# Performance work log

Hardware: AMD Instinct MI355X
Metric: run time of the kernel (lower is better)

The kernel has to match this reference:

```python
import jax, jax.numpy as jnp
import numpy as np

N_NODES = 100000
N_EDGES = 3200000
F_IN, F_HID, F_OUT = 512, 128, 32


def setup_inputs() -> dict:
    key = jax.random.key(0)
    ks = jax.random.split(key, 8)
    x = jax.random.normal(ks[0], (N_NODES, F_IN), dtype=jnp.float32)
    edge_row = jax.random.randint(ks[1], (N_EDGES,), 0, N_NODES, dtype=jnp.int32)
    edge_col = jax.random.randint(ks[2], (N_EDGES,), 0, N_NODES, dtype=jnp.int32)
    edge_val = jax.random.uniform(ks[3], (N_EDGES,), dtype=jnp.float32)
    W1 = jax.random.normal(ks[4], (F_IN, F_HID), dtype=jnp.float32) / np.sqrt(F_IN)
    b1 = jnp.zeros((F_HID,), dtype=jnp.float32)
    W2 = jax.random.normal(ks[5], (F_HID, F_OUT), dtype=jnp.float32) / np.sqrt(F_HID)
    b2 = jnp.zeros((F_OUT,), dtype=jnp.float32)
    return {"x": x, "edge_row": edge_row, "edge_col": edge_col,
            "edge_val": edge_val, "W1": W1, "b1": b1, "W2": W2, "b2": b2}


def _spmm(edge_row, edge_col, edge_val, dense):
    # out[r] = sum_{e: row[e]==r} val[e] * dense[col[e]]  (COO SpMM)
    gathered = dense[edge_col] * edge_val[:, None]  # [E, F]
    return jax.ops.segment_sum(gathered, edge_row, num_segments=N_NODES)


def reference(x, edge_row, edge_col, edge_val, W1, b1, W2, b2):
    # GraphConvolution 1: support = x@W1; out = A @ support + b1
    h = _spmm(edge_row, edge_col, edge_val, x @ W1) + b1
    h = jax.nn.relu(h)
    # GraphConvolution 2
    logits = _spmm(edge_row, edge_col, edge_val, h @ W2) + b2
    return jax.nn.log_softmax(logits, axis=1)
```

## Files before the change

kernel.cpp:

```cpp
#include <hip/hip_runtime.h>


#define NN 100000
#define NE 3200000
#define FIN 512
#define FHID 128
#define FOUT 32
#define BROWS 256
#define NBUCK 391
#define NPART 256
#define CHUNK 12800
#define TOT (NBUCK * NPART)
#define NSCAN1 98
#define GG1 ((NN + 127) / 128)

typedef __attribute__((ext_vector_type(8))) short bf16x8;
typedef __attribute__((ext_vector_type(4))) float f32x4;

static __device__ __forceinline__ unsigned short f2bf(float f) {
    unsigned u = __float_as_uint(f);
    unsigned r = (u + 0x7FFFu + ((u >> 16) & 1u)) >> 16;
    return (unsigned short)r;
}
static __device__ __forceinline__ float bf2f(unsigned short u) {
    return __uint_as_float(((unsigned)u) << 16);
}
static __device__ __forceinline__ float bflo(unsigned u) {
    return __uint_as_float(u << 16);
}
static __device__ __forceinline__ float bfhi(unsigned u) {
    return __uint_as_float(u & 0xffff0000u);
}

__global__ __launch_bounds__(256) void fused_prep_hist(const float* __restrict__ W1,
                                                       unsigned short* __restrict__ W1t,
                                                       const int* __restrict__ erow,
                                                       int* __restrict__ cntG) {
    if (blockIdx.x < NPART) {
        __shared__ int c[NBUCK];
        const int t = threadIdx.x;
        const int w = blockIdx.x;
        for (int i = t; i < NBUCK; i += 256) c[i] = 0;
        __syncthreads();
        const int e0 = w * CHUNK;
        const int e1 = min(e0 + CHUNK, NE);
        for (int e = e0 + t; e < e1; e += 256) atomicAdd(&c[erow[e] >> 8], 1);
        __syncthreads();
        for (int i = t; i < NBUCK; i += 256) cntG[w * NBUCK + i] = c[i];
    } else {
        int t = (blockIdx.x - NPART) * 256 + threadIdx.x;
        int n = t & 127;
        int k = t >> 7;
        W1t[n * 512 + k] = f2bf(W1[k * 128 + n]);
    }
}

__global__ __launch_bounds__(256) void scan1_kernel(const int* __restrict__ cntG,
                                                    int* __restrict__ off,
                                                    int* __restrict__ partials) {
    __shared__ int s[256];
    int t = threadIdx.x;
    int i0 = blockIdx.x * 1024 + t * 4;
    int v[4];
#pragma unroll
    for (int j = 0; j < 4; ++j) {
        int i = i0 + j;
        v[j] = (i < TOT) ? cntG[(i & (NPART - 1)) * NBUCK + (i >> 8)] : 0;
    }
    int lsum = v[0] + v[1] + v[2] + v[3];
    s[t] = lsum;
    __syncthreads();
    for (int o = 1; o < 256; o <<= 1) {
        int xv = (t >= o) ? s[t - o] : 0;
        __syncthreads();
        s[t] += xv;
        __syncthreads();
    }
    if (t == 255) partials[blockIdx.x] = s[255];
    int run = s[t] - lsum;
#pragma unroll
    for (int j = 0; j < 4; ++j) {
        if (i0 + j < TOT) off[i0 + j] = run;
        run += v[j];
    }
}

__global__ void scan2_kernel(int* partials) {
    __shared__ int s[128];
    int t = threadIdx.x;
    int v = (t < NSCAN1) ? partials[t] : 0;
    s[t] = v;
    __syncthreads();
    for (int o = 1; o < 128; o <<= 1) {
        int xv = (t >= o) ? s[t - o] : 0;
        __syncthreads();
        s[t] += xv;
        __syncthreads();
    }
    if (t < NSCAN1) partials[t] = s[t] - v;
}

__global__ __launch_bounds__(256) void scan3_kernel(int* __restrict__ off,
                                                    const int* __restrict__ partials) {
    int add = partials[blockIdx.x];
    int i0 = blockIdx.x * 1024 + threadIdx.x * 4;
#pragma unroll
    for (int j = 0; j < 4; ++j)
        if (i0 + j < TOT) off[i0 + j] += add;
}

__global__ __launch_bounds__(256) void scatter_part(const int* __restrict__ erow,
                                                    const int* __restrict__ ecol,
                                                    const float* __restrict__ eval,
                                                    const int* __restrict__ off,
                                                    int2* __restrict__ bcolval) {
    __shared__ int pos[NBUCK];
    const int t = threadIdx.x;
    const int w = blockIdx.x;
    for (int b = t; b < NBUCK; b += 256) pos[b] = off[b * NPART + w];
    __syncthreads();
    const int e0 = w * CHUNK;
    const int e1 = min(e0 + CHUNK, NE);
    for (int e = e0 + t; e < e1; e += 256) {
        int r = erow[e];
        int idx = atomicAdd(&pos[r >> 8], 1);
        bcolval[idx] = make_int2(ecol[e] | ((r & 255) << 20), __float_as_int(eval[e]));
    }
}

__global__ __launch_bounds__(256) void fused_csr_gemm1(
    const int* __restrict__ off, const int2* __restrict__ bcolval,
    int* __restrict__ rowptr, int2* __restrict__ epack,
    const float* __restrict__ x, const unsigned short* __restrict__ W1t,
    unsigned short* __restrict__ outd) {
    if (blockIdx.x < GG1) {
        __shared__ __align__(16) unsigned short As[128 * 32];
        const int tid = threadIdx.x;
        const int lane = tid & 63;
        const int w = __builtin_amdgcn_readfirstlane(tid >> 6);
        const int quad = lane >> 4;
        const int m = lane & 15;
        const int row0 = blockIdx.x * 128;

        f32x4 acc[8][2];
#pragma unroll
        for (int mt = 0; mt < 8; ++mt)
#pragma unroll
            for (int nt = 0; nt < 2; ++nt) acc[mt][nt] = (f32x4){0.f, 0.f, 0.f, 0.f};

        int srow[4], skq[4];
        const float* sptr[4];
#pragma unroll
        for (int s = 0; s < 4; ++s) {
            int f = tid + s * 256;
            srow[s] = f >> 3;
            skq[s] = f & 7;
            sptr[s] = x + (size_t)(row0 + srow[s]) * FIN + skq[s] * 4;
        }
        float4 ld[4];
#pragma unroll
        for (int s = 0; s < 4; ++s)
            ld[s] = (row0 + srow[s] < NN) ? *(const float4*)sptr[s]
                                          : make_float4(0.f, 0.f, 0.f, 0.f);

        for (int ks = 0; ks < 16; ++ks) {
            __syncthreads();
#pragma unroll
            for (int s = 0; s < 4; ++s) {
                int r = srow[s], kq = skq[s];
                int mt = r >> 4, mm = r & 15;
                int offs = mt * 512 + (kq >> 1) * 128 + mm * 8 + (kq & 1) * 4;
                ushort4 p;
                p.x = f2bf(ld[s].x);
                p.y = f2bf(ld[s].y);
                p.z = f2bf(ld[s].z);
                p.w = f2bf(ld[s].w);
                *(ushort4*)&As[offs] = p;
            }
            __syncthreads();
            if (ks < 15) {
#pragma unroll
                for (int s = 0; s < 4; ++s)
                    ld[s] = (row0 + srow[s] < NN)
                                ? *(const float4*)(sptr[s] + (ks + 1) * 32)
                                : make_float4(0.f, 0.f, 0.f, 0.f);
            }
            bf16x8 bfr[2];
#pragma unroll
            for (int nt = 0; nt < 2; ++nt) {
                int n = (w * 2 + nt) * 16 + m;
                bfr[nt] = *(const bf16x8*)(W1t + (size_t)n * 512 + ks * 32 + quad * 8);
            }
#pragma unroll
            for (int mt = 0; mt < 8; ++mt) {
                bf16x8 af = *(const bf16x8*)&As[mt * 512 + quad * 128 + m * 8];
                acc[mt][0] = __builtin_amdgcn_mfma_f32_16x16x32_bf16(af, bfr[0], acc[mt][0], 0, 0, 0);
                acc[mt][1] = __builtin_amdgcn_mfma_f32_16x16x32_bf16(af, bfr[1], acc[mt][1], 0, 0, 0);
            }
        }
#pragma unroll
        for (int mt = 0; mt < 8; ++mt)
#pragma unroll
            for (int nt = 0; nt < 2; ++nt) {
                int col = (w * 2 + nt) * 16 + m;
#pragma unroll
                for (int r = 0; r < 4; ++r) {
                    int row = row0 + mt * 16 + quad * 4 + r;
                    if (row < NN) outd[(size_t)row * FHID + col] = f2bf(acc[mt][nt][r]);
                }
            }
    } else {
        __shared__ int cnt[256];
        __shared__ int pos[256];
        __shared__ int s[256];
        const int b = blockIdx.x - GG1;
        const int t = threadIdx.x;
        const int s0 = off[b * NPART];
        const int send = (b == NBUCK - 1) ? NE : off[(b + 1) * NPART];
        const int n = send - s0;
        cnt[t] = 0;
        __syncthreads();
        for (int i = t; i < n; i += 256)
            atomicAdd(&cnt[((unsigned)bcolval[s0 + i].x) >> 20], 1);
        __syncthreads();
        int myc = cnt[t];
        s[t] = myc;
        __syncthreads();
        for (int o = 1; o < 256; o <<= 1) {
            int xv = (t >= o) ? s[t - o] : 0;
            __syncthreads();
            s[t] += xv;
            __syncthreads();
        }
        int excl = s[t] - myc;
        pos[t] = excl;
        int row = b * BROWS + t;
        if (row < NN) rowptr[row] = s0 + excl;
        if (b == 0 && t == 0) rowptr[NN] = NE;
        __syncthreads();
        for (int i = t; i < n; i += 256) {
            int2 v = bcolval[s0 + i];
            int p = atomicAdd(&pos[((unsigned)v.x) >> 20], 1);
            epack[s0 + p] = make_int2(v.x & 0xFFFFF, v.y);
        }
    }
}

__global__ __launch_bounds__(256) void spmm1_kernel(const int* __restrict__ rowptr,
                                                    const int2* __restrict__ epack,
                                                    const unsigned short* __restrict__ dense,
                                                    const float* __restrict__ b1,
                                                    unsigned short* __restrict__ h) {
    const int lane = threadIdx.x & 63;
    const int row = blockIdx.x * 4 + (threadIdx.x >> 6);
    const int start = __builtin_amdgcn_readfirstlane(rowptr[row]);
    const int cnt = __builtin_amdgcn_readfirstlane(rowptr[row + 1]) - start;
    const int sl16 = lane & 15;
    float acc0 = 0.f, acc1 = 0.f;

    for (int j = 0; j < cnt; j += 16) {
        int idx = j + sl16;
        idx = idx < cnt ? idx : cnt - 1;
        const int2 p = epack[start + idx];
        const int rem = cnt - j;
        unsigned d[16];
#pragma unroll
        for (int k = 0; k < 16; ++k) {
            int col = __builtin_amdgcn_readlane(p.x, k);
            col = (k < rem) ? col : 0;
            d[k] = *((const unsigned*)(dense + ((size_t)col << 7)) + lane);
        }
#pragma unroll
        for (int k = 0; k < 16; ++k) {
            float v = (k < rem) ? __int_as_float(__builtin_amdgcn_readlane(p.y, k)) : 0.f;
            acc0 = fmaf(v, bflo(d[k]), acc0);
            acc1 = fmaf(v, bfhi(d[k]), acc1);
        }
    }
    float2 bb = *(const float2*)(b1 + lane * 2);
    unsigned r0 = f2bf(fmaxf(acc0 + bb.x, 0.f));
    unsigned r1 = f2bf(fmaxf(acc1 + bb.y, 0.f));
    *((unsigned*)(h + (size_t)row * FHID) + lane) = r0 | (r1 << 16);
}

__global__ __launch_bounds__(256) void gemm2_kernel(const unsigned short* __restrict__ h,
                                                    const float* __restrict__ W2,
                                                    unsigned short* __restrict__ out) {
    __shared__ float hs[64][129];
    const int tid = threadIdx.x;
    const int lane = tid & 63;
    const int cg = __builtin_amdgcn_readfirstlane(tid >> 6);
    const int row0 = blockIdx.x * 64;
    const int row = row0 + lane;

    float acc[8];
#pragma unroll
    for (int c = 0; c < 8; ++c) acc[c] = 0.f;

#pragma unroll
    for (int j = 0; j < 8; ++j) {
        int f4 = tid + j * 256;
        int r = f4 >> 5;
        int kq = f4 & 31;
        ushort4 v = make_ushort4(0, 0, 0, 0);
        if (row0 + r < NN) v = *(const ushort4*)(h + (size_t)(row0 + r) * FHID + kq * 4);
        hs[r][kq * 4 + 0] = bf2f(v.x);
        hs[r][kq * 4 + 1] = bf2f(v.y);
        hs[r][kq * 4 + 2] = bf2f(v.z);
        hs[r][kq * 4 + 3] = bf2f(v.w);
    }
    __syncthreads();
#pragma unroll 4
    for (int k = 0; k < FHID; ++k) {
        float a = hs[lane][k];
        const float* wrow = W2 + k * FOUT + cg * 8;
#pragma unroll
        for (int c = 0; c < 8; ++c) acc[c] += a * wrow[c];
    }
    if (row < NN) {
        uint4 st;
        st.x = (unsigned)f2bf(acc[0]) | ((unsigned)f2bf(acc[1]) << 16);
        st.y = (unsigned)f2bf(acc[2]) | ((unsigned)f2bf(acc[3]) << 16);
        st.z = (unsigned)f2bf(acc[4]) | ((unsigned)f2bf(acc[5]) << 16);
        st.w = (unsigned)f2bf(acc[6]) | ((unsigned)f2bf(acc[7]) << 16);
        *(uint4*)(out + (size_t)row * FOUT + cg * 8) = st;
    }
}

__global__ __launch_bounds__(256) void spmm2_kernel(const int* __restrict__ rowptr,
                                                    const int2* __restrict__ epack,
                                                    const unsigned short* __restrict__ dense,
                                                    const float* __restrict__ b2,
                                                    float* __restrict__ out) {
    const int lane = threadIdx.x & 63;
    const int row = blockIdx.x * 4 + (threadIdx.x >> 6);
    const int start = __builtin_amdgcn_readfirstlane(rowptr[row]);
    const int cnt = __builtin_amdgcn_readfirstlane(rowptr[row + 1]) - start;
    const int col = lane & 31;
    const int slot = lane >> 5;
    const int sl16 = lane & 15;
    float acc = 0.f;

    for (int j = 0; j < cnt; j += 16) {
        int idx = j + sl16;
        idx = idx < cnt ? idx : cnt - 1;
        const int2 p = epack[start + idx];
        const int rem = cnt - j;
        unsigned short d[8];
        float vv[8];
#pragma unroll
        for (int k = 0; k < 8; ++k) {
            int cA = __builtin_amdgcn_readlane(p.x, 2 * k);
            int cB = __builtin_amdgcn_readlane(p.x, 2 * k + 1);
            int ei = 2 * k + slot;
            int c = slot ? cB : cA;
            c = (ei < rem) ? c : 0;
            d[k] = *(dense + (size_t)c * FOUT + col);
            int vA = __builtin_amdgcn_readlane(p.y, 2 * k);
            int vB = __builtin_amdgcn_readlane(p.y, 2 * k + 1);
            float v = __int_as_float(slot ? vB : vA);
            vv[k] = (ei < rem) ? v : 0.f;
        }
#pragma unroll
        for (int k = 0; k < 8; ++k) acc = fmaf(vv[k], bf2f(d[k]), acc);
    }
    acc += __shfl_xor(acc, 32, 64);
    acc += b2[col];
    float m = acc;
#pragma unroll
    for (int mask = 16; mask >= 1; mask >>= 1) m = fmaxf(m, __shfl_xor(m, mask, 64));
    float ex = expf(acc - m);
    float ssum = ex;
#pragma unroll
    for (int mask = 16; mask >= 1; mask >>= 1) ssum += __shfl_xor(ssum, mask, 64);
    float lse = m + logf(ssum);
    if (lane < 32) out[(size_t)row * FOUT + col] = acc - lse;
}

extern "C" void kernel_launch(void* const* d_in, const int* in_sizes, int n_in,
                              void* d_out, int out_size, void* d_ws, size_t ws_size,
                              hipStream_t stream) {
    const float* x = (const float*)d_in[0];
    const int* erow = (const int*)d_in[1];
    const int* ecol = (const int*)d_in[2];
    const float* eval = (const float*)d_in[3];
    const float* W1 = (const float*)d_in[4];
    const float* b1 = (const float*)d_in[5];
    const float* W2 = (const float*)d_in[6];
    const float* b2 = (const float*)d_in[7];
    float* out = (float*)d_out;

    char* ws = (char*)d_ws;
    size_t off_b = 0;
    auto walloc = [&](size_t bytes) -> void* {
        void* p = ws + off_b;
        off_b = (off_b + bytes + 255) & ~(size_t)255;
        return p;
    };
    int2* epack = (int2*)walloc((size_t)NE * 8);
    int* rowptr = (int*)walloc((size_t)(NN + 1) * 4);
    int* cntG = (int*)walloc((size_t)TOT * 4);
    int* off = (int*)walloc((size_t)TOT * 4);
    int* partials = (int*)walloc(4096);
    unsigned short* W1t = (unsigned short*)walloc((size_t)FHID * FIN * 2);
    int2* bcolval = (int2*)walloc((size_t)NE * 8);
    unsigned short* support1 = (unsigned short*)walloc((size_t)NN * FHID * 2);
    unsigned short* h = (unsigned short*)walloc((size_t)NN * FHID * 2);
    unsigned short* support2 = support1;

    fused_prep_hist<<<NPART + 256, 256, 0, stream>>>(W1, W1t, erow, cntG);
    scan1_kernel<<<NSCAN1, 256, 0, stream>>>(cntG, off, partials);
    scan2_kernel<<<1, 128, 0, stream>>>(partials);
    scan3_kernel<<<NSCAN1, 256, 0, stream>>>(off, partials);
    scatter_part<<<NPART, 256, 0, stream>>>(erow, ecol, eval, off, bcolval);
    fused_csr_gemm1<<<GG1 + NBUCK, 256, 0, stream>>>(off, bcolval, rowptr, epack,
                                                     x, W1t, support1);
    spmm1_kernel<<<NN / 4, 256, 0, stream>>>(rowptr, epack, support1, b1, h);
    gemm2_kernel<<<(NN + 63) / 64, 256, 0, stream>>>(h, W2, support2);
    spmm2_kernel<<<NN / 4, 256, 0, stream>>>(rowptr, epack, support2, b2, out);
}
```

Before: 662.3 us.

## Use finer row buckets and more partitions; schedule CSR blocks before GEMM blocks

Shrinks each row bucket from 256 to 64 rows and doubles the number of edge partitions. This gives many more, smaller CSR-build blocks, and the scans and index math are adjusted to match. The fused CSR/GEMM1 kernel now places the bucket-sort blocks first so the latency-bound sorting starts early and overlaps with the GEMM blocks. The cost is a larger offsets table and scan, with a 1024-thread second scan stage, and some idle threads in the 64-row local scan.

```diff
diff --git a/kernel.cpp b/kernel.cpp
--- a/kernel.cpp
+++ b/kernel.cpp
@@ -6,12 +6,12 @@
 #define FIN 512
 #define FHID 128
 #define FOUT 32
-#define BROWS 256
-#define NBUCK 391
-#define NPART 256
-#define CHUNK 12800
+#define BROWS 64
+#define NBUCK 1563
+#define NPART 512
+#define CHUNK 6250
 #define TOT (NBUCK * NPART)
-#define NSCAN1 98
+#define NSCAN1 782
 #define GG1 ((NN + 127) / 128)
 
 typedef __attribute__((ext_vector_type(8))) short bf16x8;
@@ -44,7 +44,7 @@
         __syncthreads();
         const int e0 = w * CHUNK;
         const int e1 = min(e0 + CHUNK, NE);
-        for (int e = e0 + t; e < e1; e += 256) atomicAdd(&c[erow[e] >> 8], 1);
+        for (int e = e0 + t; e < e1; e += 256) atomicAdd(&c[erow[e] >> 6], 1);
         __syncthreads();
         for (int i = t; i < NBUCK; i += 256) cntG[w * NBUCK + i] = c[i];
     } else {
@@ -65,7 +65,7 @@
 #pragma unroll
     for (int j = 0; j < 4; ++j) {
         int i = i0 + j;
-        v[j] = (i < TOT) ? cntG[(i & (NPART - 1)) * NBUCK + (i >> 8)] : 0;
+        v[j] = (i < TOT) ? cntG[(i & (NPART - 1)) * NBUCK + (i >> 9)] : 0;
     }
     int lsum = v[0] + v[1] + v[2] + v[3];
     s[t] = lsum;
@@ -85,13 +85,13 @@
     }
 }
 
-__global__ void scan2_kernel(int* partials) {
-    __shared__ int s[128];
+__global__ __launch_bounds__(1024) void scan2_kernel(int* partials) {
+    __shared__ int s[1024];
     int t = threadIdx.x;
     int v = (t < NSCAN1) ? partials[t] : 0;
     s[t] = v;
     __syncthreads();
-    for (int o = 1; o < 128; o <<= 1) {
+    for (int o = 1; o < 1024; o <<= 1) {
         int xv = (t >= o) ? s[t - o] : 0;
         __syncthreads();
         s[t] += xv;
@@ -123,8 +123,8 @@
     const int e1 = min(e0 + CHUNK, NE);
     for (int e = e0 + t; e < e1; e += 256) {
         int r = erow[e];
-        int idx = atomicAdd(&pos[r >> 8], 1);
-        bcolval[idx] = make_int2(ecol[e] | ((r & 255) << 20), __float_as_int(eval[e]));
+        int idx = atomicAdd(&pos[r >> 6], 1);
+        bcolval[idx] = make_int2(ecol[e] | ((r & 63) << 20), __float_as_int(eval[e]));
     }
 }
 
@@ -133,14 +133,14 @@
     int* __restrict__ rowptr, int2* __restrict__ epack,
     const float* __restrict__ x, const unsigned short* __restrict__ W1t,
     unsigned short* __restrict__ outd) {
-    if (blockIdx.x < GG1) {
+    if (blockIdx.x >= NBUCK) {
         __shared__ __align__(16) unsigned short As[128 * 32];
         const int tid = threadIdx.x;
         const int lane = tid & 63;
         const int w = __builtin_amdgcn_readfirstlane(tid >> 6);
         const int quad = lane >> 4;
         const int m = lane & 15;
-        const int row0 = blockIdx.x * 128;
+        const int row0 = (blockIdx.x - NBUCK) * 128;
 
         f32x4 acc[8][2];
 #pragma unroll
@@ -210,32 +210,34 @@
                 }
             }
     } else {
-        __shared__ int cnt[256];
-        __shared__ int pos[256];
-        __shared__ int s[256];
-        const int b = blockIdx.x - GG1;
+        __shared__ int cnt[BROWS];
+        __shared__ int pos[BROWS];
+        __shared__ int s[BROWS];
+        const int b = blockIdx.x;
         const int t = threadIdx.x;
         const int s0 = off[b * NPART];
         const int send = (b == NBUCK - 1) ? NE : off[(b + 1) * NPART];
         const int n = send - s0;
-        cnt[t] = 0;
+        if (t < BROWS) cnt[t] = 0;
         __syncthreads();
         for (int i = t; i < n; i += 256)
             atomicAdd(&cnt[((unsigned)bcolval[s0 + i].x) >> 20], 1);
         __syncthreads();
-        int myc = cnt[t];
-        s[t] = myc;
-        __syncthreads();
-        for (int o = 1; o < 256; o <<= 1) {
-            int xv = (t >= o) ? s[t - o] : 0;
+        int myc = (t < BROWS) ? cnt[t] : 0;
+        if (t < BROWS) s[t] = myc;
+        __syncthreads();
+        for (int o = 1; o < BROWS; o <<= 1) {
+            int xv = (t >= o && t < BROWS) ? s[t - o] : 0;
             __syncthreads();
-            s[t] += xv;
+            if (t < BROWS) s[t] += xv;
             __syncthreads();
         }
-        int excl = s[t] - myc;
-        pos[t] = excl;
-        int row = b * BROWS + t;
-        if (row < NN) rowptr[row] = s0 + excl;
+        if (t < BROWS) {
+            int excl = s[t] - myc;
+            pos[t] = excl;
+            int row = b * BROWS + t;
+            if (row < NN) rowptr[row] = s0 + excl;
+        }
         if (b == 0 && t == 0) rowptr[NN] = NE;
         __syncthreads();
         for (int i = t; i < n; i += 256) {
@@ -410,10 +412,10 @@
 
     fused_prep_hist<<<NPART + 256, 256, 0, stream>>>(W1, W1t, erow, cntG);
     scan1_kernel<<<NSCAN1, 256, 0, stream>>>(cntG, off, partials);
-    scan2_kernel<<<1, 128, 0, stream>>>(partials);
+    scan2_kernel<<<1, 1024, 0, stream>>>(partials);
     scan3_kernel<<<NSCAN1, 256, 0, stream>>>(off, partials);
     scatter_part<<<NPART, 256, 0, stream>>>(erow, ecol, eval, off, bcolval);
-    fused_csr_gemm1<<<GG1 + NBUCK, 256, 0, stream>>>(off, bcolval, rowptr, epack,
+    fused_csr_gemm1<<<NBUCK + GG1, 256, 0, stream>>>(off, bcolval, rowptr, epack,
                                                      x, W1t, support1);
     spmm1_kernel<<<NN / 4, 256, 0, stream>>>(rowptr, epack, support1, b1, h);
     gemm2_kernel<<<(NN + 63) / 64, 256, 0, stream>>>(h, W2, support2);
```

Measured after the change: 663.7 us. Within noise of the previous version (+0.2%).
